# Kernel tuning notes

Measured on AMD Instinct MI355X. Metric: run time of the kernel, lower is better.

Reference implementation:

```python
import jax, jax.numpy as jnp
import numpy as np

H = 4  # num_heads
K = 16  # model_k
EPS = 1e-5


def layernorm(x, g, b):
    m = jnp.mean(x, axis=-1, keepdims=True)
    v = jnp.mean(jnp.square(x - m), axis=-1, keepdims=True)
    return (x - m) * jax.lax.rsqrt(v + EPS) * g + b


def setup_inputs() -> dict:
    key = jax.random.key(0)
    ks = jax.random.split(key, 12)
    B, N, C, NN = 4, 8192, 256, 32
    s = 0.02
    return {
        "xyz": jax.random.normal(ks[0], (B, N, 2), jnp.float32),
        "xy_embed": jax.random.normal(ks[1], (B, N, C), jnp.float32),
        "nns": jax.random.randint(ks[2], (B, N, NN), 0, N),
        "ln1_g": jnp.ones((C,), jnp.float32),
        "ln1_b": jnp.zeros((C,), jnp.float32),
        "w_qkv": jax.random.normal(ks[3], (C, 3 * C), jnp.float32) * s,
        "w_d1": jax.random.normal(ks[4], (2, C), jnp.float32) * s,
        "b_d1": jnp.zeros((C,), jnp.float32),
        "w_d2": jax.random.normal(ks[5], (C, C), jnp.float32) * s,
        "b_d2": jnp.zeros((C,), jnp.float32),
        "w_proj": jax.random.normal(ks[6], (C, C), jnp.float32) * s,
        "b_proj": jnp.zeros((C,), jnp.float32),
        "ln2_g": jnp.ones((C,), jnp.float32),
        "ln2_b": jnp.zeros((C,), jnp.float32),
        "w_m1": jax.random.normal(ks[7], (C, 4 * C), jnp.float32) * s,
        "b_m1": jnp.zeros((4 * C,), jnp.float32),
        "w_m2": jax.random.normal(ks[8], (4 * C, C), jnp.float32) * s,
        "b_m2": jnp.zeros((C,), jnp.float32),
    }


def reference(xyz, xy_embed, nns, ln1_g, ln1_b, w_qkv, w_d1, b_d1, w_d2, b_d2,
              w_proj, b_proj, ln2_g, ln2_b, w_m1, b_m1, w_m2, b_m2):
    B, N, C = xy_embed.shape
    hd = C // H
    knn = nns[:, :, :K]  # [B, N, K]
    bidx = jnp.arange(B)[:, None, None]

    # --- Attention on norm1(xy_embed) ---
    h = layernorm(xy_embed, ln1_g, ln1_b)
    qkv = h @ w_qkv  # [B, N, 3C]
    q, kf, vf = jnp.split(qkv, 3, axis=-1)

    kk = kf[bidx, knn]  # gather: [B, N, K, C]
    vv = vf[bidx, knn]  # [B, N, K, C]
    xy_knn = xyz[bidx, knn]  # [B, N, K, 2]

    # relative position encoding MLP
    rel = xyz[:, :, None, :] - xy_knn  # [B, N, K, 2]
    pe = jax.nn.relu(rel @ w_d1 + b_d1) @ w_d2 + b_d2  # [B, N, K, C]

    # split heads (channel-chunk split, matching torch reshape semantics)
    qh = q.reshape(B, N, H, hd).transpose(0, 2, 1, 3)          # [B,H,N,hd]
    kh = kk.reshape(B, N, K, H, hd).transpose(0, 3, 1, 2, 4)   # [B,H,N,K,hd]
    vh = vv.reshape(B, N, K, H, hd).transpose(0, 3, 1, 2, 4)
    peh = pe.reshape(B, N, K, H, hd).transpose(0, 3, 1, 2, 4)

    attn = jnp.einsum('bhnd,bhnkd->bhnk', qh, kh) / np.sqrt(hd).astype(np.float32)
    attn = jax.nn.softmax(attn, axis=-1)  # [B,H,N,K]

    x = jnp.einsum('bhnk,bhnkd->bhnd', attn, vh + peh)  # [B,H,N,hd]
    x = x.transpose(0, 2, 1, 3).reshape(B, N, C)
    x = x @ w_proj + b_proj

    # residual + MLP block
    x = xy_embed + x
    h2 = layernorm(x, ln2_g, ln2_b)
    mlp = jax.nn.gelu(h2 @ w_m1 + b_m1, approximate=False) @ w_m2 + b_m2
    x = x + mlp
    return x
```

## Files before the change

### kernel.cpp

```cpp
#include <hip/hip_runtime.h>
#include <hip/hip_bf16.h>
#include <math.h>

#define NPTS 8192
#define BDIM 4
#define BN   32768
#define CDIM 256
#define KNN  16
#define NNCOL 32

typedef __attribute__((ext_vector_type(8))) short short8_t;
typedef __attribute__((ext_vector_type(4))) float f32x4;

__device__ __forceinline__ ushort bf16_rne(float f) {
  unsigned int u = __float_as_uint(f);
  u += 0x7fffu + ((u >> 16) & 1u);
  return (ushort)(u >> 16);
}
__device__ __forceinline__ void bf16_split(float f, ushort& h, ushort& l) {
  unsigned int u = __float_as_uint(f);
  h = (ushort)(u >> 16);
  float fh = __uint_as_float(u & 0xffff0000u);
  l = (ushort)(__float_as_uint(f - fh) >> 16);
}
__device__ __forceinline__ float bf16_tof(ushort h) {
  return __uint_as_float(((unsigned int)h) << 16);
}
__device__ __forceinline__ float gelu_exact(float z) {
  return 0.5f * z * (1.0f + erff(z * 0.70710678118654752f));
}

__global__ __launch_bounds__(256) void wsplit_kernel(
    const float* __restrict__ in, ushort* __restrict__ oh,
    ushort* __restrict__ ol, int R, int Cc) {
  __shared__ float tile[32][33];
  const int tx = threadIdx.x & 31, ty = threadIdx.x >> 5;
  const int r0 = blockIdx.y * 32, c0 = blockIdx.x * 32;
  #pragma unroll
  for (int i = 0; i < 4; i++)
    tile[ty + 8 * i][tx] = in[(size_t)(r0 + ty + 8 * i) * Cc + c0 + tx];
  __syncthreads();
  #pragma unroll
  for (int i = 0; i < 4; i++) {
    const int cc = ty + 8 * i;
    ushort h, l;
    bf16_split(tile[tx][cc], h, l);
    oh[(size_t)(c0 + cc) * R + r0 + tx] = h;
    ol[(size_t)(c0 + cc) * R + r0 + tx] = l;
  }
}

__global__ __launch_bounds__(256) void ln_apply_kernel(
    const float* __restrict__ x, const float* __restrict__ g,
    const float* __restrict__ b, ushort* __restrict__ oh,
    ushort* __restrict__ ol) {
  const int row = blockIdx.x * 4 + (threadIdx.x >> 6);
  const int l = threadIdx.x & 63;
  const float4 v = *(const float4*)(x + (size_t)row * CDIM + l * 4);
  float s  = v.x + v.y + v.z + v.w;
  float sq = v.x * v.x + v.y * v.y + v.z * v.z + v.w * v.w;
  #pragma unroll
  for (int off = 1; off < 64; off <<= 1) {
    s  += __shfl_xor(s, off);
    sq += __shfl_xor(sq, off);
  }
  const float m = s * (1.0f / 256.0f);
  const float r = rsqrtf(sq * (1.0f / 256.0f) - m * m + 1e-5f);
  const float4 gv = *(const float4*)(g + l * 4);
  const float4 bv = *(const float4*)(b + l * 4);
  const float y0 = (v.x - m) * r * gv.x + bv.x;
  const float y1 = (v.y - m) * r * gv.y + bv.y;
  const float y2 = (v.z - m) * r * gv.z + bv.z;
  const float y3 = (v.w - m) * r * gv.w + bv.w;
  ushort4 hv, lv;
  bf16_split(y0, hv.x, lv.x); bf16_split(y1, hv.y, lv.y);
  bf16_split(y2, hv.z, lv.z); bf16_split(y3, hv.w, lv.w);
  *(ushort4*)(oh + (size_t)row * CDIM + l * 4) = hv;
  *(ushort4*)(ol + (size_t)row * CDIM + l * 4) = lv;
}

template <int EPI>
__global__ __launch_bounds__(256) void gemm_bf3(
    const ushort* __restrict__ AH, const ushort* __restrict__ AL,
    const ushort* __restrict__ BH, const ushort* __restrict__ BL,
    const float* __restrict__ bias, float* __restrict__ Cf,
    ushort* __restrict__ CH, ushort* __restrict__ CL,
    const float* __restrict__ res, int M, int Nn, int Kk) {
  __shared__ __align__(16) ushort AsH[128 * 32];
  __shared__ __align__(16) ushort AsL[128 * 32];
  __shared__ __align__(16) ushort BsH[128 * 32];
  __shared__ __align__(16) ushort BsL[128 * 32];

  const int t = threadIdx.x;
  const int w = t >> 6;
  const int l = t & 63;
  const int la = l & 15;
  const int lb = l >> 4;
  const int wr = w >> 1;
  const int wc = w & 1;
  const int m0 = blockIdx.y * 128;
  const int n0 = blockIdx.x * 128;

  f32x4 acc[4][4];
  #pragma unroll
  for (int i = 0; i < 4; i++)
    #pragma unroll
    for (int j = 0; j < 4; j++) acc[i][j] = (f32x4){0.f, 0.f, 0.f, 0.f};

  for (int k0 = 0; k0 < Kk; k0 += 32) {
    #pragma unroll
    for (int gi = 0; gi < 2; gi++) {
      const int g = t + gi * 256;
      const int row = g >> 2;
      const int kg = (g & 3) * 8;
      const int lds_off = row * 32 + (kg ^ ((row & 3) << 3));
      const size_t ga = (size_t)(m0 + row) * Kk + k0 + kg;
      const size_t gb = (size_t)(n0 + row) * Kk + k0 + kg;
      *(short8_t*)&AsH[lds_off] = *(const short8_t*)(AH + ga);
      *(short8_t*)&AsL[lds_off] = *(const short8_t*)(AL + ga);
      *(short8_t*)&BsH[lds_off] = *(const short8_t*)(BH + gb);
      *(short8_t*)&BsL[lds_off] = *(const short8_t*)(BL + gb);
    }
    __syncthreads();

    short8_t aH[4], aL[4], bH[4], bL[4];
    #pragma unroll
    for (int i = 0; i < 4; i++) {
      const int row = wr * 64 + i * 16 + la;
      const int off = row * 32 + ((lb * 8) ^ ((row & 3) << 3));
      aH[i] = *(const short8_t*)&AsH[off];
      aL[i] = *(const short8_t*)&AsL[off];
    }
    #pragma unroll
    for (int j = 0; j < 4; j++) {
      const int row = wc * 64 + j * 16 + la;
      const int off = row * 32 + ((lb * 8) ^ ((row & 3) << 3));
      bH[j] = *(const short8_t*)&BsH[off];
      bL[j] = *(const short8_t*)&BsL[off];
    }
    #pragma unroll
    for (int i = 0; i < 4; i++)
      #pragma unroll
      for (int j = 0; j < 4; j++) {
        acc[i][j] = __builtin_amdgcn_mfma_f32_16x16x32_bf16(aH[i], bH[j], acc[i][j], 0, 0, 0);
        acc[i][j] = __builtin_amdgcn_mfma_f32_16x16x32_bf16(aH[i], bL[j], acc[i][j], 0, 0, 0);
        acc[i][j] = __builtin_amdgcn_mfma_f32_16x16x32_bf16(aL[i], bH[j], acc[i][j], 0, 0, 0);
      }
    __syncthreads();
  }

  const int colBase = n0 + wc * 64 + la;
  float biasv[4] = {0.f, 0.f, 0.f, 0.f};
  if (EPI >= 2) {
    #pragma unroll
    for (int j = 0; j < 4; j++) biasv[j] = bias[colBase + j * 16];
  }
  #pragma unroll
  for (int i = 0; i < 4; i++) {
    #pragma unroll
    for (int r = 0; r < 4; r++) {
      const int row = m0 + wr * 64 + i * 16 + lb * 4 + r;
      #pragma unroll
      for (int j = 0; j < 4; j++) {
        const int col = colBase + j * 16;
        float o = acc[i][j][r] + biasv[j];
        if (EPI == 0) {
          CH[(size_t)row * Nn + col] = bf16_rne(o);
        } else if (EPI == 2) {
          o += res[(size_t)row * Nn + col];
          Cf[(size_t)row * Nn + col] = o;
        } else {
          o = gelu_exact(o);
          ushort h, lo2;
          bf16_split(o, h, lo2);
          CH[(size_t)row * Nn + col] = h;
          CL[(size_t)row * Nn + col] = lo2;
        }
      }
    }
  }
}

__global__ __launch_bounds__(256) void attn_kernel(
    const ushort* __restrict__ qkv, const int* __restrict__ nns,
    const float* __restrict__ xyz, const float* __restrict__ w_d1,
    const float* __restrict__ b_d1, const ushort* __restrict__ W2H,
    const float* __restrict__ b_d2, ushort* __restrict__ outH,
    ushort* __restrict__ outL) {
  __shared__ __align__(16) ushort s_lds[32 * 256];
  __shared__ __align__(16) float ov_lds[8][256];
  __shared__ float a_lds[8][64];

  const int t = threadIdx.x;
  const int w = t >> 6;
  const int l = t & 63;
  const int h = l >> 4;
  const int j16 = l & 15;
  const int c0 = l * 4;
  const int blk = blockIdx.x;

  const float4 w10 = *(const float4*)(w_d1 + c0);
  const float4 w11 = *(const float4*)(w_d1 + 256 + c0);
  const float4 b1v = *(const float4*)(b_d1 + c0);
  const float4 b2v = *(const float4*)(b_d2 + c0);

  for (int pl = 0; pl < 2; pl++) {
    const int p  = w * 2 + pl;
    const int gp = blk * 8 + p;
    const int b  = gp >> 13;

    const float2 xy0 = *(const float2*)(xyz + gp * 2);

    int rowj[KNN];
    #pragma unroll
    for (int j = 0; j < KNN; j++) rowj[j] = (b << 13) + nns[gp * NNCOL + j];

    const size_t qbase = (size_t)gp * 768 + (h << 6);
    const size_t kbase = (size_t)rowj[j16] * 768 + 256 + (h << 6);
    float d = 0.f;
    #pragma unroll
    for (int u = 0; u < 8; u++) {
      const short8_t qv = *(const short8_t*)(qkv + qbase + u * 8);
      const short8_t kv = *(const short8_t*)(qkv + kbase + u * 8);
      #pragma unroll
      for (int e = 0; e < 8; e++)
        d += bf16_tof((ushort)qv[e]) * bf16_tof((ushort)kv[e]);
    }
    const float myscore = d * 0.125f;

    float mx = myscore;
    mx = fmaxf(mx, __shfl_xor(mx, 1)); mx = fmaxf(mx, __shfl_xor(mx, 2));
    mx = fmaxf(mx, __shfl_xor(mx, 4)); mx = fmaxf(mx, __shfl_xor(mx, 8));
    const float e = __expf(myscore - mx);
    float sum = e;
    sum += __shfl_xor(sum, 1); sum += __shfl_xor(sum, 2);
    sum += __shfl_xor(sum, 4); sum += __shfl_xor(sum, 8);
    a_lds[p][l] = e / sum;
    __syncthreads();

    float sacc[4][4] = {};
    float4 ov = {0.f, 0.f, 0.f, 0.f};
    #pragma unroll
    for (int j = 0; j < KNN; j++) {
      const int r = rowj[j];
      const ushort4 vu = *(const ushort4*)(qkv + (size_t)r * 768 + 512 + c0);
      const float v0 = bf16_tof(vu.x), v1 = bf16_tof(vu.y);
      const float v2 = bf16_tof(vu.z), v3 = bf16_tof(vu.w);
      const float2 xyj = *(const float2*)(xyz + r * 2);
      const float rx = xy0.x - xyj.x;
      const float ry = xy0.y - xyj.y;
      const float u0 = fmaxf(rx * w10.x + ry * w11.x + b1v.x, 0.f);
      const float u1 = fmaxf(rx * w10.y + ry * w11.y + b1v.y, 0.f);
      const float u2 = fmaxf(rx * w10.z + ry * w11.z + b1v.z, 0.f);
      const float u3 = fmaxf(rx * w10.w + ry * w11.w + b1v.w, 0.f);
      const float a0 = a_lds[p][0 * 16 + j];
      const float a1 = a_lds[p][1 * 16 + j];
      const float a2 = a_lds[p][2 * 16 + j];
      const float a3 = a_lds[p][3 * 16 + j];
      sacc[0][0] += a0 * u0; sacc[0][1] += a0 * u1; sacc[0][2] += a0 * u2; sacc[0][3] += a0 * u3;
      sacc[1][0] += a1 * u0; sacc[1][1] += a1 * u1; sacc[1][2] += a1 * u2; sacc[1][3] += a1 * u3;
      sacc[2][0] += a2 * u0; sacc[2][1] += a2 * u1; sacc[2][2] += a2 * u2; sacc[2][3] += a2 * u3;
      sacc[3][0] += a3 * u0; sacc[3][1] += a3 * u1; sacc[3][2] += a3 * u2; sacc[3][3] += a3 * u3;
      const float aown = a_lds[p][(h << 4) + j];
      ov.x += aown * v0; ov.y += aown * v1;
      ov.z += aown * v2; ov.w += aown * v3;
    }
    #pragma unroll
    for (int hh = 0; hh < 4; hh++) {
      const int row = p * 4 + hh;
      ushort4 sv;
      sv.x = bf16_rne(sacc[hh][0]); sv.y = bf16_rne(sacc[hh][1]);
      sv.z = bf16_rne(sacc[hh][2]); sv.w = bf16_rne(sacc[hh][3]);
      *(ushort4*)&s_lds[row * 256 + (c0 ^ ((row & 15) << 3))] = sv;
    }
    float4 ovw;
    ovw.x = ov.x + b2v.x; ovw.y = ov.y + b2v.y;
    ovw.z = ov.z + b2v.z; ovw.w = ov.w + b2v.w;
    *(float4*)&ov_lds[p][c0] = ovw;
  }
  __syncthreads();

  const int la = l & 15;
  const int lb = l >> 4;
  f32x4 acc2[2][4];
  #pragma unroll
  for (int mf = 0; mf < 2; mf++)
    #pragma unroll
    for (int nf = 0; nf < 4; nf++) acc2[mf][nf] = (f32x4){0.f, 0.f, 0.f, 0.f};

  #pragma unroll
  for (int ks = 0; ks < 8; ks++) {
    const int k8 = lb * 8 + ks * 32;
    short8_t av[2], bv[4];
    #pragma unroll
    for (int mf = 0; mf < 2; mf++) {
      const int row = mf * 16 + la;
      av[mf] = *(const short8_t*)&s_lds[row * 256 + (k8 ^ ((row & 15) << 3))];
    }
    #pragma unroll
    for (int nf = 0; nf < 4; nf++) {
      const int n = (w << 6) + nf * 16 + la;
      bv[nf] = *(const short8_t*)(W2H + (size_t)n * 256 + k8);
    }
    #pragma unroll
    for (int mf = 0; mf < 2; mf++)
      #pragma unroll
      for (int nf = 0; nf < 4; nf++)
        acc2[mf][nf] = __builtin_amdgcn_mfma_f32_16x16x32_bf16(
            av[mf], bv[nf], acc2[mf][nf], 0, 0, 0);
  }

  #pragma unroll
  for (int mf = 0; mf < 2; mf++) {
    const int p = mf * 4 + lb;
    const size_t gp = (size_t)(blk * 8 + p);
    #pragma unroll
    for (int nf = 0; nf < 4; nf++) {
      const int c = (w << 6) + nf * 16 + la;
      float pe;
      if (w == 0)      pe = acc2[mf][nf][0];
      else if (w == 1) pe = acc2[mf][nf][1];
      else if (w == 2) pe = acc2[mf][nf][2];
      else             pe = acc2[mf][nf][3];
      const float o = pe + ov_lds[p][c];
      ushort hv, lv;
      bf16_split(o, hv, lv);
      outH[gp * 256 + c] = hv;
      outL[gp * 256 + c] = lv;
    }
  }
}

extern "C" void kernel_launch(void* const* d_in, const int* in_sizes, int n_in,
                              void* d_out, int out_size, void* d_ws,
                              size_t ws_size, hipStream_t stream) {
  const float* xyz      = (const float*)d_in[0];
  const float* xy_embed = (const float*)d_in[1];
  const int*   nns      = (const int*)d_in[2];
  const float* ln1_g    = (const float*)d_in[3];
  const float* ln1_b    = (const float*)d_in[4];
  const float* w_qkv    = (const float*)d_in[5];
  const float* w_d1     = (const float*)d_in[6];
  const float* b_d1     = (const float*)d_in[7];
  const float* w_d2     = (const float*)d_in[8];
  const float* b_d2     = (const float*)d_in[9];
  const float* w_proj   = (const float*)d_in[10];
  const float* b_proj   = (const float*)d_in[11];
  const float* ln2_g    = (const float*)d_in[12];
  const float* ln2_b    = (const float*)d_in[13];
  const float* w_m1     = (const float*)d_in[14];
  const float* b_m1     = (const float*)d_in[15];
  const float* w_m2     = (const float*)d_in[16];
  const float* b_m2     = (const float*)d_in[17];
  float* out = (float*)d_out;

  char* ws = (char*)d_ws;
  const size_t MB = 1024 * 1024;
  ushort* qkv_bf = (ushort*)(ws);
  ushort* midH   = (ushort*)(ws);
  ushort* midL   = (ushort*)(ws + 32 * MB);
  ushort* attnH  = (ushort*)(ws + 48 * MB);
  ushort* attnL  = (ushort*)(ws + 64 * MB);
  ushort* lnH    = (ushort*)(ws + 80 * MB);
  ushort* lnL    = (ushort*)(ws + 96 * MB);
  ushort* wbase  = (ushort*)(ws + 112 * MB);
  ushort* WqH  = wbase;             ushort* WqL  = WqH + 768 * 256;
  ushort* WpH  = WqL + 768 * 256;   ushort* WpL  = WpH + 256 * 256;
  ushort* Wm1H = WpL + 256 * 256;   ushort* Wm1L = Wm1H + 1024 * 256;
  ushort* Wm2H = Wm1L + 1024 * 256; ushort* Wm2L = Wm2H + 256 * 1024;
  ushort* W2H  = Wm2L + 256 * 1024; ushort* W2L  = W2H + 256 * 256;

  wsplit_kernel<<<dim3(768 / 32, 256 / 32), 256, 0, stream>>>(w_qkv, WqH, WqL, 256, 768);
  wsplit_kernel<<<dim3(256 / 32, 256 / 32), 256, 0, stream>>>(w_proj, WpH, WpL, 256, 256);
  wsplit_kernel<<<dim3(1024 / 32, 256 / 32), 256, 0, stream>>>(w_m1, Wm1H, Wm1L, 256, 1024);
  wsplit_kernel<<<dim3(256 / 32, 1024 / 32), 256, 0, stream>>>(w_m2, Wm2H, Wm2L, 1024, 256);
  wsplit_kernel<<<dim3(256 / 32, 256 / 32), 256, 0, stream>>>(w_d2, W2H, W2L, 256, 256);

  ln_apply_kernel<<<BN / 4, 256, 0, stream>>>(xy_embed, ln1_g, ln1_b, lnH, lnL);

  gemm_bf3<0><<<dim3(768 / 128, BN / 128), 256, 0, stream>>>(
      lnH, lnL, WqH, WqL, nullptr, nullptr, qkv_bf, nullptr, nullptr, BN, 768, 256);

  attn_kernel<<<BN / 8, 256, 0, stream>>>(qkv_bf, nns, xyz, w_d1, b_d1, W2H,
                                          b_d2, attnH, attnL);

  gemm_bf3<2><<<dim3(256 / 128, BN / 128), 256, 0, stream>>>(
      attnH, attnL, WpH, WpL, b_proj, out, nullptr, nullptr, xy_embed, BN, 256, 256);

  ln_apply_kernel<<<BN / 4, 256, 0, stream>>>(out, ln2_g, ln2_b, lnH, lnL);

  const int CHUNK = 16384;
  for (int ch = 0; ch < BN / CHUNK; ch++) {
    float* xrow = out + (size_t)ch * CHUNK * 256;
    gemm_bf3<3><<<dim3(1024 / 128, CHUNK / 128), 256, 0, stream>>>(
        lnH + (size_t)ch * CHUNK * 256, lnL + (size_t)ch * CHUNK * 256,
        Wm1H, Wm1L, b_m1, nullptr, midH, midL, nullptr, CHUNK, 1024, 256);
    gemm_bf3<2><<<dim3(256 / 128, CHUNK / 128), 256, 0, stream>>>(
        midH, midL, Wm2H, Wm2L, b_m2, xrow, nullptr, nullptr, xrow, CHUNK, 256, 1024);
  }
}
```

Baseline: 611.1 us.

## Prepack w_d2 into MFMA fragment order and coalesce attention output stores

Adds a kernel that converts w_d2 to bf16 laid out in MFMA B-fragment order, so each lane in the attention kernel reads one contiguous 16-byte chunk instead of strided rows. The per-point __syncthreads after the softmax is removed. The epilogue now accumulates the PE result into the shared ov buffer and writes the output with fully coalesced row stores, and launch bounds request 4 blocks per SM. Removing the barrier relies on each wave reading only its own a_lds entries, and the simplified swizzle (row<<3) has to stay within bounds for rows up to 31.

After: 661.9 us. +8.3%, slower.

```diff
diff --git a/kernel.cpp b/kernel.cpp
--- a/kernel.cpp
+++ b/kernel.cpp
@@ -48,6 +48,22 @@
     oh[(size_t)(c0 + cc) * R + r0 + tx] = h;
     ol[(size_t)(c0 + cc) * R + r0 + tx] = l;
   }
+}
+
+__global__ __launch_bounds__(256) void w2frag_kernel(
+    const float* __restrict__ w_d2, ushort* __restrict__ W2F) {
+  const int tid = blockIdx.x * 256 + threadIdx.x;
+  const int l  = tid & 63;
+  const int nf = (tid >> 6) & 3;
+  const int ks = (tid >> 8) & 7;
+  const int h  = tid >> 11;
+  const int n  = h * 64 + nf * 16 + (l & 15);
+  const int k0 = ks * 32 + (l >> 4) * 8;
+  ushort out[8];
+  #pragma unroll
+  for (int e = 0; e < 8; e++) out[e] = bf16_rne(w_d2[(size_t)(k0 + e) * 256 + n]);
+  *(ushort4*)(W2F + (size_t)tid * 8)     = *(ushort4*)&out[0];
+  *(ushort4*)(W2F + (size_t)tid * 8 + 4) = *(ushort4*)&out[4];
 }
 
 __global__ __launch_bounds__(256) void ln_apply_kernel(
@@ -181,10 +197,10 @@
   }
 }
 
-__global__ __launch_bounds__(256) void attn_kernel(
+__global__ __launch_bounds__(256, 4) void attn_kernel(
     const ushort* __restrict__ qkv, const int* __restrict__ nns,
     const float* __restrict__ xyz, const float* __restrict__ w_d1,
-    const float* __restrict__ b_d1, const ushort* __restrict__ W2H,
+    const float* __restrict__ b_d1, const ushort* __restrict__ W2F,
     const float* __restrict__ b_d2, ushort* __restrict__ outH,
     ushort* __restrict__ outL) {
   __shared__ __align__(16) ushort s_lds[32 * 256];
@@ -236,7 +252,6 @@
     sum += __shfl_xor(sum, 1); sum += __shfl_xor(sum, 2);
     sum += __shfl_xor(sum, 4); sum += __shfl_xor(sum, 8);
     a_lds[p][l] = e / sum;
-    __syncthreads();
 
     float sacc[4][4] = {};
     float4 ov = {0.f, 0.f, 0.f, 0.f};
@@ -271,7 +286,7 @@
       ushort4 sv;
       sv.x = bf16_rne(sacc[hh][0]); sv.y = bf16_rne(sacc[hh][1]);
       sv.z = bf16_rne(sacc[hh][2]); sv.w = bf16_rne(sacc[hh][3]);
-      *(ushort4*)&s_lds[row * 256 + (c0 ^ ((row & 15) << 3))] = sv;
+      *(ushort4*)&s_lds[row * 256 + (c0 ^ (row << 3))] = sv;
     }
     float4 ovw;
     ovw.x = ov.x + b2v.x; ovw.y = ov.y + b2v.y;
@@ -291,29 +306,24 @@
   #pragma unroll
   for (int ks = 0; ks < 8; ks++) {
     const int k8 = lb * 8 + ks * 32;
-    short8_t av[2], bv[4];
+    short8_t av[2];
     #pragma unroll
     for (int mf = 0; mf < 2; mf++) {
-      const int row = mf * 16 + la;
-      av[mf] = *(const short8_t*)&s_lds[row * 256 + (k8 ^ ((row & 15) << 3))];
+      const int arow = mf * 16 + la;
+      av[mf] = *(const short8_t*)&s_lds[arow * 256 + (k8 ^ (arow << 3))];
     }
     #pragma unroll
     for (int nf = 0; nf < 4; nf++) {
-      const int n = (w << 6) + nf * 16 + la;
-      bv[nf] = *(const short8_t*)(W2H + (size_t)n * 256 + k8);
-    }
-    #pragma unroll
-    for (int mf = 0; mf < 2; mf++)
-      #pragma unroll
-      for (int nf = 0; nf < 4; nf++)
-        acc2[mf][nf] = __builtin_amdgcn_mfma_f32_16x16x32_bf16(
-            av[mf], bv[nf], acc2[mf][nf], 0, 0, 0);
+      const short8_t bv = *(const short8_t*)(
+          W2F + ((size_t)(((w * 8 + ks) * 4 + nf) * 64 + l)) * 8);
+      acc2[0][nf] = __builtin_amdgcn_mfma_f32_16x16x32_bf16(av[0], bv, acc2[0][nf], 0, 0, 0);
+      acc2[1][nf] = __builtin_amdgcn_mfma_f32_16x16x32_bf16(av[1], bv, acc2[1][nf], 0, 0, 0);
+    }
   }
 
   #pragma unroll
   for (int mf = 0; mf < 2; mf++) {
-    const int p = mf * 4 + lb;
-    const size_t gp = (size_t)(blk * 8 + p);
+    const int p2 = mf * 4 + lb;
     #pragma unroll
     for (int nf = 0; nf < 4; nf++) {
       const int c = (w << 6) + nf * 16 + la;
@@ -322,12 +332,19 @@
       else if (w == 1) pe = acc2[mf][nf][1];
       else if (w == 2) pe = acc2[mf][nf][2];
       else             pe = acc2[mf][nf][3];
-      const float o = pe + ov_lds[p][c];
-      ushort hv, lv;
-      bf16_split(o, hv, lv);
-      outH[gp * 256 + c] = hv;
-      outL[gp * 256 + c] = lv;
-    }
+      ov_lds[p2][c] += pe;
+    }
+  }
+  __syncthreads();
+
+  const int gp0 = blk * 8;
+  #pragma unroll
+  for (int p = 0; p < 8; p++) {
+    const float o = ov_lds[p][t];
+    ushort hv, lv;
+    bf16_split(o, hv, lv);
+    outH[(size_t)(gp0 + p) * 256 + t] = hv;
+    outL[(size_t)(gp0 + p) * 256 + t] = lv;
   }
 }
 
@@ -368,20 +385,20 @@
   ushort* WpH  = WqL + 768 * 256;   ushort* WpL  = WpH + 256 * 256;
   ushort* Wm1H = WpL + 256 * 256;   ushort* Wm1L = Wm1H + 1024 * 256;
   ushort* Wm2H = Wm1L + 1024 * 256; ushort* Wm2L = Wm2H + 256 * 1024;
-  ushort* W2H  = Wm2L + 256 * 1024; ushort* W2L  = W2H + 256 * 256;
+  ushort* W2F  = Wm2L + 256 * 1024;
 
   wsplit_kernel<<<dim3(768 / 32, 256 / 32), 256, 0, stream>>>(w_qkv, WqH, WqL, 256, 768);
   wsplit_kernel<<<dim3(256 / 32, 256 / 32), 256, 0, stream>>>(w_proj, WpH, WpL, 256, 256);
   wsplit_kernel<<<dim3(1024 / 32, 256 / 32), 256, 0, stream>>>(w_m1, Wm1H, Wm1L, 256, 1024);
   wsplit_kernel<<<dim3(256 / 32, 1024 / 32), 256, 0, stream>>>(w_m2, Wm2H, Wm2L, 1024, 256);
-  wsplit_kernel<<<dim3(256 / 32, 256 / 32), 256, 0, stream>>>(w_d2, W2H, W2L, 256, 256);
+  w2frag_kernel<<<32, 256, 0, stream>>>(w_d2, W2F);
 
   ln_apply_kernel<<<BN / 4, 256, 0, stream>>>(xy_embed, ln1_g, ln1_b, lnH, lnL);
 
   gemm_bf3<0><<<dim3(768 / 128, BN / 128), 256, 0, stream>>>(
       lnH, lnL, WqH, WqL, nullptr, nullptr, qkv_bf, nullptr, nullptr, BN, 768, 256);
 
-  attn_kernel<<<BN / 8, 256, 0, stream>>>(qkv_bf, nns, xyz, w_d1, b_d1, W2H,
+  attn_kernel<<<BN / 8, 256, 0, stream>>>(qkv_bf, nns, xyz, w_d1, b_d1, W2F,
                                           b_d2, attnH, attnL);
 
   gemm_bf3<2><<<dim3(256 / 128, BN / 128), 256, 0, stream>>>(
```
